# Kernel optimization log

Hardware: AMD Instinct MI355X
Metric: run time of the kernel (lower is better)

The kernel has to match this reference:

```python
import jax, jax.numpy as jnp
import numpy as np

N = 50000
E = 800000
F = 64
OUT = 64
K = 3


def setup_inputs() -> dict:
    key = jax.random.key(0)
    k1, k2, k3, k4, k5, k6 = jax.random.split(key, 6)
    x = jax.random.normal(k1, (N, F), dtype=jnp.float32)
    edge_row = jax.random.randint(k2, (E,), 0, N, dtype=jnp.int32)
    edge_col = jax.random.randint(k3, (E,), 0, N, dtype=jnp.int32)
    # positive edge weights (e.g., normalized adjacency values)
    edge_val = jax.random.uniform(k4, (E,), dtype=jnp.float32)
    W = jax.random.normal(k5, (F * (K + 1), OUT), dtype=jnp.float32) / np.sqrt(F * (K + 1))
    b = jax.random.normal(k6, (OUT,), dtype=jnp.float32) * 0.01
    return {"x": x, "edge_row": edge_row, "edge_col": edge_col,
            "edge_val": edge_val, "W": W, "b": b}


def _spmm(edge_row, edge_col, edge_val, h, n):
    # row i of adj @ h : sum over edges (i, j, v) of v * h[j]
    return jax.ops.segment_sum(edge_val[:, None] * h[edge_col], edge_row,
                               num_segments=n)


def reference(x, edge_row, edge_col, edge_val, W, b):
    out = x
    xs = [x]
    for _ in range(K):
        out = _spmm(edge_row, edge_col, edge_val, out, N)
        xs.append(out)
    h = jnp.concatenate(xs, axis=-1)  # [N, F*(K+1)]
    return h @ W + b
```

## Files before the change

### kernel.cpp

```cpp
#include <hip/hip_runtime.h>


#define F 64
#define OUT 64
#define SCAN_ELEMS 1024

__global__ __launch_bounds__(256) void count_rows(
    const int* __restrict__ row, int* __restrict__ counts, int E) {
  int e = blockIdx.x * 256 + threadIdx.x;
  if (e < E) atomicAdd(&counts[row[e]], 1);
}

__global__ __launch_bounds__(256) void block_scan(
    const int* __restrict__ counts, int* __restrict__ offsets,
    int* __restrict__ blockSums, int N) {
  __shared__ int s[256];
  int t = threadIdx.x;
  int base = blockIdx.x * SCAN_ELEMS + t * 4;
  int v0 = 0, v1 = 0, v2 = 0, v3 = 0;
  if (base + 3 < N) {
    int4 c = *(const int4*)&counts[base];
    v0 = c.x; v1 = c.y; v2 = c.z; v3 = c.w;
  } else {
    if (base < N)     v0 = counts[base];
    if (base + 1 < N) v1 = counts[base + 1];
    if (base + 2 < N) v2 = counts[base + 2];
  }
  s[t] = v0 + v1 + v2 + v3;
  __syncthreads();
  for (int d = 1; d < 256; d <<= 1) {
    int x = (t >= d) ? s[t - d] : 0;
    __syncthreads();
    s[t] += x;
    __syncthreads();
  }
  int ex = (t == 0) ? 0 : s[t - 1];
  if (t == 255) blockSums[blockIdx.x] = s[255];
  int o0 = ex, o1 = o0 + v0, o2 = o1 + v1, o3 = o2 + v2;
  if (base + 3 < N) {
    *(int4*)&offsets[base] = make_int4(o0, o1, o2, o3);
  } else {
    if (base < N)     offsets[base]     = o0;
    if (base + 1 < N) offsets[base + 1] = o1;
    if (base + 2 < N) offsets[base + 2] = o2;
  }
}

__global__ __launch_bounds__(64) void scan_sums(int* __restrict__ blockSums, int nb) {
  int lane = threadIdx.x;
  if (nb <= 64) {
    int v = (lane < nb) ? blockSums[lane] : 0;
    int incl = v;
    for (int d = 1; d < 64; d <<= 1) {
      int u = __shfl_up(incl, d, 64);
      if (lane >= d) incl += u;
    }
    if (lane < nb) blockSums[lane] = incl - v;
  } else if (lane == 0) {
    int run = 0;
    for (int i = 0; i < nb; ++i) { int c = blockSums[i]; blockSums[i] = run; run += c; }
  }
}

__global__ __launch_bounds__(256) void add_offsets(
    int* __restrict__ offsets, const int* __restrict__ blockSums,
    int* __restrict__ cursor, int N, int E) {
  int i = blockIdx.x * 256 + threadIdx.x;
  if (i < N) {
    int o = offsets[i] + blockSums[i >> 10];
    offsets[i] = o;
    cursor[i] = o;
  }
  if (i == 0) offsets[N] = E;
}

__global__ __launch_bounds__(256) void scatter_edges(
    const int* __restrict__ row, const int* __restrict__ col,
    const float* __restrict__ val, int* __restrict__ cursor,
    float2* __restrict__ recs, int E) {
  int e = blockIdx.x * 256 + threadIdx.x;
  if (e < E) {
    int r = row[e];
    int p = atomicAdd(&cursor[r], 1);
    recs[p] = make_float2(__int_as_float(col[e]), val[e]);
  }
}

__global__ __launch_bounds__(256) void spmm_rec4(
    const int* __restrict__ off, const float2* __restrict__ recs,
    const float* __restrict__ hin, float* __restrict__ hout, int N) {
  int r = blockIdx.x * 4 + (threadIdx.x >> 6);
  if (r >= N) return;
  int lane = threadIdx.x & 63;
  int g = lane >> 4;
  int fp = (lane & 15) << 2;
  int i = off[r], end = off[r + 1];
  float4 acc = make_float4(0.f, 0.f, 0.f, 0.f);

  int bb = i + g;
  for (; bb + 4 < end; bb += 8) {
    float2 e0 = recs[bb];
    float2 e1 = recs[bb + 4];
    float4 h0 = *(const float4*)&hin[(size_t)__float_as_int(e0.x) * F + fp];
    float4 h1 = *(const float4*)&hin[(size_t)__float_as_int(e1.x) * F + fp];
    acc.x = fmaf(e0.y, h0.x, acc.x);
    acc.y = fmaf(e0.y, h0.y, acc.y);
    acc.z = fmaf(e0.y, h0.z, acc.z);
    acc.w = fmaf(e0.y, h0.w, acc.w);
    acc.x = fmaf(e1.y, h1.x, acc.x);
    acc.y = fmaf(e1.y, h1.y, acc.y);
    acc.z = fmaf(e1.y, h1.z, acc.z);
    acc.w = fmaf(e1.y, h1.w, acc.w);
  }
  if (bb < end) {
    float2 e0 = recs[bb];
    float4 h0 = *(const float4*)&hin[(size_t)__float_as_int(e0.x) * F + fp];
    acc.x = fmaf(e0.y, h0.x, acc.x);
    acc.y = fmaf(e0.y, h0.y, acc.y);
    acc.z = fmaf(e0.y, h0.z, acc.z);
    acc.w = fmaf(e0.y, h0.w, acc.w);
  }

  acc.x += __shfl_xor(acc.x, 16, 64);
  acc.y += __shfl_xor(acc.y, 16, 64);
  acc.z += __shfl_xor(acc.z, 16, 64);
  acc.w += __shfl_xor(acc.w, 16, 64);
  acc.x += __shfl_xor(acc.x, 32, 64);
  acc.y += __shfl_xor(acc.y, 32, 64);
  acc.z += __shfl_xor(acc.z, 32, 64);
  acc.w += __shfl_xor(acc.w, 32, 64);

  if (g == 0) *(float4*)&hout[(size_t)r * F + fp] = acc;
}

__global__ __launch_bounds__(256) void gemm_fused4_v2(
    const float* __restrict__ h0, const float* __restrict__ h1,
    const float* __restrict__ h2, const float* __restrict__ W,
    const float* __restrict__ bias, float* __restrict__ out, int N) {
  __shared__ float Ws[64 * 64];
  const float* hs[4] = {h0, h1, h2, out};

  int nl = threadIdx.x >> 2;
  int oq = threadIdx.x & 3;
  int og = oq << 4;
  int node = blockIdx.x * 64 + nl;
  int nodec = min(node, N - 1);

  const float4* b4 = (const float4*)bias;
  float4 a0 = b4[oq * 4 + 0];
  float4 a1 = b4[oq * 4 + 1];
  float4 a2 = b4[oq * 4 + 2];
  float4 a3 = b4[oq * 4 + 3];

  for (int s = 0; s < 4; ++s) {
    __syncthreads();
    const float4* Wg = (const float4*)(W + s * 4096);
#pragma unroll
    for (int i = 0; i < 4; ++i)
      ((float4*)Ws)[threadIdx.x + i * 256] = Wg[threadIdx.x + i * 256];
    __syncthreads();

    const float* hrow = hs[s] + (size_t)nodec * F;
#pragma unroll 4
    for (int k4 = 0; k4 < 16; ++k4) {
      float4 h4 = *(const float4*)&hrow[k4 * 4];
#pragma unroll
      for (int j = 0; j < 4; ++j) {
        float hv = (j == 0) ? h4.x : (j == 1) ? h4.y : (j == 2) ? h4.z : h4.w;
        const float4* w4 = (const float4*)&Ws[(k4 * 4 + j) * 64 + og];
        float4 w0 = w4[0], w1 = w4[1], w2 = w4[2], w3 = w4[3];
        a0.x = fmaf(hv, w0.x, a0.x); a0.y = fmaf(hv, w0.y, a0.y);
        a0.z = fmaf(hv, w0.z, a0.z); a0.w = fmaf(hv, w0.w, a0.w);
        a1.x = fmaf(hv, w1.x, a1.x); a1.y = fmaf(hv, w1.y, a1.y);
        a1.z = fmaf(hv, w1.z, a1.z); a1.w = fmaf(hv, w1.w, a1.w);
        a2.x = fmaf(hv, w2.x, a2.x); a2.y = fmaf(hv, w2.y, a2.y);
        a2.z = fmaf(hv, w2.z, a2.z); a2.w = fmaf(hv, w2.w, a2.w);
        a3.x = fmaf(hv, w3.x, a3.x); a3.y = fmaf(hv, w3.y, a3.y);
        a3.z = fmaf(hv, w3.z, a3.z); a3.w = fmaf(hv, w3.w, a3.w);
      }
    }
  }

  if (node < N) {
    float4* o4 = (float4*)&out[(size_t)node * OUT + og];
    o4[0] = a0; o4[1] = a1; o4[2] = a2; o4[3] = a3;
  }
}

extern "C" void kernel_launch(void* const* d_in, const int* in_sizes, int n_in,
                              void* d_out, int out_size, void* d_ws, size_t ws_size,
                              hipStream_t stream) {
  const float* x    = (const float*)d_in[0];
  const int*   erow = (const int*)d_in[1];
  const int*   ecol = (const int*)d_in[2];
  const float* eval = (const float*)d_in[3];
  const float* W    = (const float*)d_in[4];
  const float* b    = (const float*)d_in[5];
  float* out = (float*)d_out;

  int N = in_sizes[0] / F;
  int E = in_sizes[1];
  size_t SZ = (size_t)N * F * sizeof(float);
  int nScanBlocks = (N + SCAN_ELEMS - 1) / SCAN_ELEMS;

  char* p = (char*)d_ws;
  float*  hA     = (float*)p;  p += SZ;
  float*  hB     = (float*)p;  p += SZ;
  float2* recs   = (float2*)p; p += (size_t)E * sizeof(float2);
  int*    counts = (int*)p;    p += (size_t)N * sizeof(int);
  int*    offs   = (int*)p;    p += (size_t)(N + 1) * sizeof(int);
  int*    cursor = (int*)p;    p += (size_t)N * sizeof(int);
  int*    bsums  = (int*)p;    p += (size_t)nScanBlocks * sizeof(int);

  int egrid = (E + 255) / 256;
  int sgrid = (N + 3) / 4;
  int ggrid = (N + 63) / 64;

  hipMemsetAsync(counts, 0, (size_t)N * sizeof(int), stream);
  count_rows<<<egrid, 256, 0, stream>>>(erow, counts, E);
  block_scan<<<nScanBlocks, 256, 0, stream>>>(counts, offs, bsums, N);
  scan_sums<<<1, 64, 0, stream>>>(bsums, nScanBlocks);
  add_offsets<<<(N + 255) / 256, 256, 0, stream>>>(offs, bsums, cursor, N, E);
  scatter_edges<<<egrid, 256, 0, stream>>>(erow, ecol, eval, cursor, recs, E);

  spmm_rec4<<<sgrid, 256, 0, stream>>>(offs, recs, x, hA, N);
  spmm_rec4<<<sgrid, 256, 0, stream>>>(offs, recs, hA, hB, N);
  spmm_rec4<<<sgrid, 256, 0, stream>>>(offs, recs, hB, out, N);

  gemm_fused4_v2<<<ggrid, 256, 0, stream>>>(x, hA, hB, W, b, out, N);
}
```

Measured before the change: 232.9 us.

## Partition edge scatter by row range and map one 16-lane group per row in SpMM

Result: faster. 217.8 us (-6.5%).

```diff
diff --git a/kernel.cpp b/kernel.cpp
--- a/kernel.cpp
+++ b/kernel.cpp
@@ -4,6 +4,7 @@
 #define F 64
 #define OUT 64
 #define SCAN_ELEMS 1024
+#define NPART 8
 
 __global__ __launch_bounds__(256) void count_rows(
     const int* __restrict__ row, int* __restrict__ counts, int E) {
@@ -74,63 +75,51 @@
   if (i == 0) offsets[N] = E;
 }
 
-__global__ __launch_bounds__(256) void scatter_edges(
+__global__ __launch_bounds__(256) void scatter_part(
     const int* __restrict__ row, const int* __restrict__ col,
     const float* __restrict__ val, int* __restrict__ cursor,
-    float2* __restrict__ recs, int E) {
-  int e = blockIdx.x * 256 + threadIdx.x;
-  if (e < E) {
-    int r = row[e];
-    int p = atomicAdd(&cursor[r], 1);
-    recs[p] = make_float2(__int_as_float(col[e]), val[e]);
-  }
-}
-
-__global__ __launch_bounds__(256) void spmm_rec4(
+    float2* __restrict__ recs, int E, int rpp) {
+  int part = blockIdx.x & (NPART - 1);
+  int e = (blockIdx.x >> 3) * 256 + threadIdx.x;
+  if (e >= E) return;
+  int r = row[e];
+  unsigned lo = (unsigned)(part * rpp);
+  if ((unsigned)(r - lo) >= (unsigned)rpp) return;
+  int p = atomicAdd(&cursor[r], 1);
+  recs[p] = make_float2(__int_as_float(col[e]), val[e]);
+}
+
+__global__ __launch_bounds__(256) void spmm_g16(
     const int* __restrict__ off, const float2* __restrict__ recs,
     const float* __restrict__ hin, float* __restrict__ hout, int N) {
-  int r = blockIdx.x * 4 + (threadIdx.x >> 6);
+  int r = (blockIdx.x * 256 + threadIdx.x) >> 4;
   if (r >= N) return;
-  int lane = threadIdx.x & 63;
-  int g = lane >> 4;
-  int fp = (lane & 15) << 2;
+  int fp = (threadIdx.x & 15) << 2;
   int i = off[r], end = off[r + 1];
   float4 acc = make_float4(0.f, 0.f, 0.f, 0.f);
 
-  int bb = i + g;
-  for (; bb + 4 < end; bb += 8) {
-    float2 e0 = recs[bb];
-    float2 e1 = recs[bb + 4];
+  for (; i + 4 <= end; i += 4) {
+    float2 e0 = recs[i], e1 = recs[i + 1], e2 = recs[i + 2], e3 = recs[i + 3];
     float4 h0 = *(const float4*)&hin[(size_t)__float_as_int(e0.x) * F + fp];
     float4 h1 = *(const float4*)&hin[(size_t)__float_as_int(e1.x) * F + fp];
-    acc.x = fmaf(e0.y, h0.x, acc.x);
-    acc.y = fmaf(e0.y, h0.y, acc.y);
-    acc.z = fmaf(e0.y, h0.z, acc.z);
-    acc.w = fmaf(e0.y, h0.w, acc.w);
-    acc.x = fmaf(e1.y, h1.x, acc.x);
-    acc.y = fmaf(e1.y, h1.y, acc.y);
-    acc.z = fmaf(e1.y, h1.z, acc.z);
-    acc.w = fmaf(e1.y, h1.w, acc.w);
-  }
-  if (bb < end) {
-    float2 e0 = recs[bb];
+    float4 h2 = *(const float4*)&hin[(size_t)__float_as_int(e2.x) * F + fp];
+    float4 h3 = *(const float4*)&hin[(size_t)__float_as_int(e3.x) * F + fp];
+    acc.x = fmaf(e0.y, h0.x, acc.x); acc.y = fmaf(e0.y, h0.y, acc.y);
+    acc.z = fmaf(e0.y, h0.z, acc.z); acc.w = fmaf(e0.y, h0.w, acc.w);
+    acc.x = fmaf(e1.y, h1.x, acc.x); acc.y = fmaf(e1.y, h1.y, acc.y);
+    acc.z = fmaf(e1.y, h1.z, acc.z); acc.w = fmaf(e1.y, h1.w, acc.w);
+    acc.x = fmaf(e2.y, h2.x, acc.x); acc.y = fmaf(e2.y, h2.y, acc.y);
+    acc.z = fmaf(e2.y, h2.z, acc.z); acc.w = fmaf(e2.y, h2.w, acc.w);
+    acc.x = fmaf(e3.y, h3.x, acc.x); acc.y = fmaf(e3.y, h3.y, acc.y);
+    acc.z = fmaf(e3.y, h3.z, acc.z); acc.w = fmaf(e3.y, h3.w, acc.w);
+  }
+  for (; i < end; ++i) {
+    float2 e0 = recs[i];
     float4 h0 = *(const float4*)&hin[(size_t)__float_as_int(e0.x) * F + fp];
-    acc.x = fmaf(e0.y, h0.x, acc.x);
-    acc.y = fmaf(e0.y, h0.y, acc.y);
-    acc.z = fmaf(e0.y, h0.z, acc.z);
-    acc.w = fmaf(e0.y, h0.w, acc.w);
-  }
-
-  acc.x += __shfl_xor(acc.x, 16, 64);
-  acc.y += __shfl_xor(acc.y, 16, 64);
-  acc.z += __shfl_xor(acc.z, 16, 64);
-  acc.w += __shfl_xor(acc.w, 16, 64);
-  acc.x += __shfl_xor(acc.x, 32, 64);
-  acc.y += __shfl_xor(acc.y, 32, 64);
-  acc.z += __shfl_xor(acc.z, 32, 64);
-  acc.w += __shfl_xor(acc.w, 32, 64);
-
-  if (g == 0) *(float4*)&hout[(size_t)r * F + fp] = acc;
+    acc.x = fmaf(e0.y, h0.x, acc.x); acc.y = fmaf(e0.y, h0.y, acc.y);
+    acc.z = fmaf(e0.y, h0.z, acc.z); acc.w = fmaf(e0.y, h0.w, acc.w);
+  }
+  *(float4*)&hout[(size_t)r * F + fp] = acc;
 }
 
 __global__ __launch_bounds__(256) void gemm_fused4_v2(
@@ -202,6 +191,7 @@
   int E = in_sizes[1];
   size_t SZ = (size_t)N * F * sizeof(float);
   int nScanBlocks = (N + SCAN_ELEMS - 1) / SCAN_ELEMS;
+  int rpp = (N + NPART - 1) / NPART;
 
   char* p = (char*)d_ws;
   float*  hA     = (float*)p;  p += SZ;
@@ -213,7 +203,7 @@
   int*    bsums  = (int*)p;    p += (size_t)nScanBlocks * sizeof(int);
 
   int egrid = (E + 255) / 256;
-  int sgrid = (N + 3) / 4;
+  int g16grid = ((size_t)N * 16 + 255) / 256;
   int ggrid = (N + 63) / 64;
 
   hipMemsetAsync(counts, 0, (size_t)N * sizeof(int), stream);
@@ -221,11 +211,11 @@
   block_scan<<<nScanBlocks, 256, 0, stream>>>(counts, offs, bsums, N);
   scan_sums<<<1, 64, 0, stream>>>(bsums, nScanBlocks);
   add_offsets<<<(N + 255) / 256, 256, 0, stream>>>(offs, bsums, cursor, N, E);
-  scatter_edges<<<egrid, 256, 0, stream>>>(erow, ecol, eval, cursor, recs, E);
-
-  spmm_rec4<<<sgrid, 256, 0, stream>>>(offs, recs, x, hA, N);
-  spmm_rec4<<<sgrid, 256, 0, stream>>>(offs, recs, hA, hB, N);
-  spmm_rec4<<<sgrid, 256, 0, stream>>>(offs, recs, hB, out, N);
+  scatter_part<<<egrid * NPART, 256, 0, stream>>>(erow, ecol, eval, cursor, recs, E, rpp);
+
+  spmm_g16<<<g16grid, 256, 0, stream>>>(offs, recs, x, hA, N);
+  spmm_g16<<<g16grid, 256, 0, stream>>>(offs, recs, hA, hB, N);
+  spmm_g16<<<g16grid, 256, 0, stream>>>(offs, recs, hB, out, N);
 
   gemm_fused4_v2<<<ggrid, 256, 0, stream>>>(x, hA, hB, W, b, out, N);
 }
```
